# Kernel optimization log

Measured on AMD Instinct MI355X. Metric: run time of the kernel, lower is better.

The kernel has to match this reference:

```python
import jax, jax.numpy as jnp
import numpy as np

EMBED_DIM = 584
HEADS = 8
HEAD_SIZE = EMBED_DIM // HEADS  # 73
CTX = 200


def setup_inputs() -> dict:
    key = jax.random.key(0)
    ks = jax.random.split(key, 6)
    B, T = 256, 200
    x = jax.random.normal(ks[0], (B, T, EMBED_DIM), dtype=jnp.float32)
    s = 1.0 / np.sqrt(EMBED_DIM)
    # per-head q/k/v Linear(EMBED_DIM, HEAD_SIZE, bias=False) weights, stacked: [H, hs, E]
    Wq = jax.random.uniform(ks[1], (HEADS, HEAD_SIZE, EMBED_DIM), jnp.float32, -s, s)
    Wk = jax.random.uniform(ks[2], (HEADS, HEAD_SIZE, EMBED_DIM), jnp.float32, -s, s)
    Wv = jax.random.uniform(ks[3], (HEADS, HEAD_SIZE, EMBED_DIM), jnp.float32, -s, s)
    Wo = jax.random.uniform(ks[4], (EMBED_DIM, EMBED_DIM), jnp.float32, -s, s)
    bo = jax.random.uniform(ks[5], (EMBED_DIM,), jnp.float32, -s, s)
    return {"x": x, "Wq": Wq, "Wk": Wk, "Wv": Wv, "Wo": Wo, "bo": bo}


def reference(x, Wq, Wk, Wv, Wo, bo):
    B, T, C = x.shape  # C == EMBED_DIM
    # per-head projections, batched: [B, H, T, hs]
    q = jnp.einsum('bte,hfe->bhtf', x, Wq)
    k = jnp.einsum('bte,hfe->bhtf', x, Wk)
    v = jnp.einsum('bte,hfe->bhtf', x, Wv)
    # NOTE: original scales by EMBED_DIM**-0.5 (C), not head_size**-0.5
    scores = jnp.einsum('bhtf,bhsf->bhts', q, k) * (C ** -0.5)
    causal = jnp.tril(jnp.ones((T, T), dtype=bool))
    scores = jnp.where(causal, scores, -jnp.inf)
    w = jax.nn.softmax(scores, axis=-1)
    out = jnp.einsum('bhts,bhsf->bhtf', w, v)  # [B,H,T,hs]
    out = out.transpose(0, 2, 1, 3).reshape(B, T, C)  # concat heads on last dim
    return out @ Wo.T + bo
```

## Files before the change

### kernel.cpp

```cpp
#include <hip/hip_runtime.h>

typedef __bf16 bf16x8 __attribute__((ext_vector_type(8)));
typedef __bf16 bf16x4 __attribute__((ext_vector_type(4)));
typedef float f32x4 __attribute__((ext_vector_type(4)));

#define EMBED 584
#define KP 608
#define HEADS 8
#define HS 73
#define HSQ 80
#define CTX 200
#define NBATCH 256
#define MROWS 51200
#define NQKV 1752

#define CH 112
#define KSS 104
#define VTS 136
#define PSS 136

__device__ __forceinline__ void gld_lds16(__bf16* lds, const __bf16* g) {
  __builtin_amdgcn_global_load_lds(
      (const __attribute__((address_space(1))) void*)g,
      (__attribute__((address_space(3))) void*)lds, 16, 0, 0);
}

__global__ __launch_bounds__(256) void cvt_x(const float* __restrict__ x,
                                             __bf16* __restrict__ out) {
  int i = blockIdx.x * 256 + threadIdx.x;
  int r = i / 76, slot = i - r * 76;
  int col = slot * 8;
  bf16x8 o8 = {};
  if (col < EMBED) {
    const float4* s4 = (const float4*)(x + (size_t)r * EMBED + col);
    float4 f0 = s4[0], f1 = s4[1];
    o8[0] = (__bf16)f0.x; o8[1] = (__bf16)f0.y; o8[2] = (__bf16)f0.z; o8[3] = (__bf16)f0.w;
    o8[4] = (__bf16)f1.x; o8[5] = (__bf16)f1.y; o8[6] = (__bf16)f1.z; o8[7] = (__bf16)f1.w;
  }
  *(bf16x8*)(out + (size_t)r * KP + col) = o8;
}

__global__ __launch_bounds__(256) void pack_w(const float* __restrict__ Wq,
                                              const float* __restrict__ Wk,
                                              const float* __restrict__ Wv,
                                              const float* __restrict__ Wo,
                                              __bf16* __restrict__ out) {
  int i = blockIdx.x * 256 + threadIdx.x;
  if (i >= 2336 * 76) return;
  int r = i / 76, slot = i - r * 76;
  int col = slot * 8;
  bf16x8 o8 = {};
  if (col < EMBED) {
    const float* src = r < 584  ? Wq + (size_t)r * EMBED
                     : r < 1168 ? Wk + (size_t)(r - 584) * EMBED
                     : r < 1752 ? Wv + (size_t)(r - 1168) * EMBED
                                : Wo + (size_t)(r - 1752) * EMBED;
    const float4* s4 = (const float4*)(src + col);
    float4 f0 = s4[0], f1 = s4[1];
    o8[0] = (__bf16)f0.x; o8[1] = (__bf16)f0.y; o8[2] = (__bf16)f0.z; o8[3] = (__bf16)f0.w;
    o8[4] = (__bf16)f1.x; o8[5] = (__bf16)f1.y; o8[6] = (__bf16)f1.z; o8[7] = (__bf16)f1.w;
  }
  *(bf16x8*)(out + (size_t)r * KP + col) = o8;
}

__global__ __launch_bounds__(256) void gemm_qkv(const __bf16* __restrict__ A,
                                                const __bf16* __restrict__ Bm,
                                                __bf16* __restrict__ Q,
                                                __bf16* __restrict__ Ko,
                                                __bf16* __restrict__ V) {
  __shared__ __bf16 As[2][4096];
  __shared__ __bf16 Bs[2][4096];
  int tid = threadIdx.x;
  int id = blockIdx.x;
  int idp = (id & 7) * 700 + (id >> 3);
  int bm = idp / 14, bn = idp - bm * 14;
  int wid = tid >> 6, lane = tid & 63;
  int wm = (wid & 1) * 64, wn = (wid >> 1) * 64;
  int lr = lane & 15, lq = lane >> 4;
  const __bf16* aB = A  + (size_t)(bm * 128 + wid * 32 + (lane >> 2)) * KP + (lane & 3) * 8;
  const __bf16* bB = Bm + (size_t)(bn * 128 + wid * 32 + (lane >> 2)) * KP + (lane & 3) * 8;
  f32x4 acc[4][4] = {};
  gld_lds16(As[0] + wid * 1024,       aB);
  gld_lds16(As[0] + wid * 1024 + 512, aB + 16 * KP);
  gld_lds16(Bs[0] + wid * 1024,       bB);
  gld_lds16(Bs[0] + wid * 1024 + 512, bB + 16 * KP);
  __syncthreads();
  int cur = 0;
  for (int kt = 0; kt < 19; ++kt) {
    if (kt < 18) {
      int k0 = (kt + 1) * 32;
      gld_lds16(As[cur ^ 1] + wid * 1024,       aB + k0);
      gld_lds16(As[cur ^ 1] + wid * 1024 + 512, aB + 16 * KP + k0);
      gld_lds16(Bs[cur ^ 1] + wid * 1024,       bB + k0);
      gld_lds16(Bs[cur ^ 1] + wid * 1024 + 512, bB + 16 * KP + k0);
    }
    bf16x8 af[4], bfr[4];
#pragma unroll
    for (int i = 0; i < 4; ++i)
      af[i] = *(const bf16x8*)&As[cur][(wm + i * 16 + lr) * 32 + lq * 8];
#pragma unroll
    for (int j = 0; j < 4; ++j)
      bfr[j] = *(const bf16x8*)&Bs[cur][(wn + j * 16 + lr) * 32 + lq * 8];
#pragma unroll
    for (int i = 0; i < 4; ++i)
#pragma unroll
      for (int j = 0; j < 4; ++j)
        acc[i][j] = __builtin_amdgcn_mfma_f32_16x16x32_bf16(af[i], bfr[j], acc[i][j], 0, 0, 0);
    if (kt < 18) __syncthreads();
    cur ^= 1;
  }
  int whichj[4], ojv[4];
  __bf16* Pj[4];
  bool okj[4];
#pragma unroll
  for (int j = 0; j < 4; ++j) {
    int n = bn * 128 + wn + j * 16 + lr;
    okj[j] = (n < NQKV);
    int nn = okj[j] ? n : 0;
    int which = nn / EMBED;
    int rem = nn - which * EMBED;
    int hh = rem / HS;
    int f = rem - hh * HS;
    whichj[j] = which;
    ojv[j] = (which == 2) ? (hh * 16000 + f * 200) : (hh * 16000 + f);
    Pj[j] = (which == 0) ? Q : (which == 1) ? Ko : V;
  }
#pragma unroll
  for (int i = 0; i < 4; ++i) {
    int m0 = bm * 128 + wm + i * 16 + lq * 4;
    int bb = m0 / CTX;
    int tt = m0 - bb * CTX;
    int a_qk = bb * 128000 + tt * 80;
    int a_v  = bb * 128000 + tt;
#pragma unroll
    for (int j = 0; j < 4; ++j) {
      if (!okj[j]) continue;
      if (whichj[j] == 2) {
        bf16x4 v4;
#pragma unroll
        for (int r = 0; r < 4; ++r) v4[r] = (__bf16)acc[i][j][r];
        *(bf16x4*)&Pj[j][a_v + ojv[j]] = v4;
      } else {
        int base = a_qk + ojv[j];
#pragma unroll
        for (int r = 0; r < 4; ++r)
          Pj[j][base + r * 80] = (__bf16)acc[i][j][r];
      }
    }
  }
}

__global__ __launch_bounds__(256) void attn_kernel(const __bf16* __restrict__ q,
                                                   const __bf16* __restrict__ k,
                                                   const __bf16* __restrict__ v,
                                                   __bf16* __restrict__ o) {
  __shared__ __align__(16) __bf16 lds[31232];
  __bf16* Ks = lds;
  __bf16* Vt = lds + 11648;
  __bf16* Ps = lds + 22528;

  int tid = threadIdx.x;
  int bh = blockIdx.x;
  int b = bh >> 3, h = bh & 7;
  const __bf16* qg = q + (size_t)bh * (CTX * HSQ);
  const __bf16* kg = k + (size_t)bh * (CTX * HSQ);
  const __bf16* vg = v + (size_t)bh * (HSQ * CTX);

  {
    f32x4* p = (f32x4*)lds;
    for (int i = tid; i < 3904; i += 256) p[i] = f32x4{0.f, 0.f, 0.f, 0.f};
  }
  if (h == 0) {
    bf16x8 z = {};
    for (int i = tid; i < CTX * 3; i += 256) {
      int t = i / 3, seg = i - t * 3;
      *(bf16x8*)&o[((size_t)(b * CTX + t)) * KP + EMBED + seg * 8] = z;
    }
  }
  __syncthreads();

  int wid = tid >> 6, lane = tid & 63;
  int lr = lane & 15, g = lane >> 4;
  __bf16* Pw = Ps + wid * (16 * PSS);
  const int nstr = (wid == 0) ? 4 : 3;
  const float scale = 0.04138029443264672f;

  float ml[4][4], ll[4][4];
  f32x4 ov[4][5];
#pragma unroll
  for (int i = 0; i < 4; ++i)
#pragma unroll
    for (int r = 0; r < 4; ++r) { ml[i][r] = -1e30f; ll[i][r] = 0.f; }
#pragma unroll
  for (int i = 0; i < 4; ++i)
#pragma unroll
    for (int nt = 0; nt < 5; ++nt) ov[i][nt] = f32x4{0.f, 0.f, 0.f, 0.f};

  for (int c = 0; c < 2; ++c) {
    int key0 = c * CH;
    for (int idx = tid; idx < CH * 10; idx += 256) {
      int s = idx / 10, slot = idx % 10;
      int key = key0 + s;
      if (key < CTX)
        *(bf16x8*)&Ks[s * KSS + slot * 8] =
            *(const bf16x8*)&kg[(size_t)key * HSQ + slot * 8];
    }
    for (int idx = tid; idx < HSQ * 14; idx += 256) {
      int f = idx / 14, slot = idx % 14;
      int s0 = slot * 8;
      bf16x8 vv;
      if (key0 + s0 + 7 < CTX) {
        vv = *(const bf16x8*)&vg[(size_t)f * CTX + key0 + s0];
      } else {
#pragma unroll
        for (int j = 0; j < 8; ++j)
          vv[j] = (key0 + s0 + j < CTX) ? vg[(size_t)f * CTX + key0 + s0 + j]
                                        : (__bf16)0.f;
      }
      *(bf16x8*)&Vt[f * VTS + s0] = vv;
    }
    __syncthreads();

#pragma unroll
    for (int i = 0; i < 4; ++i) {
      if (i >= nstr) break;
      int strip = wid + 4 * i;
      int row0 = strip * 16;
      bf16x8 qf[3];
      qf[0] = *(const bf16x8*)&qg[(size_t)(row0 + lr) * HSQ + g * 8];
      qf[1] = *(const bf16x8*)&qg[(size_t)(row0 + lr) * HSQ + 32 + g * 8];
      if (g < 2)
        qf[2] = *(const bf16x8*)&qg[(size_t)(row0 + lr) * HSQ + 64 + g * 8];
      else
        qf[2] = bf16x8{};
      float sc[7][4];
#pragma unroll
      for (int nt = 0; nt < 7; ++nt) {
        f32x4 acc = {};
#pragma unroll
        for (int kc = 0; kc < 3; ++kc) {
          bf16x8 kf = *(const bf16x8*)&Ks[(nt * 16 + lr) * KSS + kc * 32 + g * 8];
          acc = __builtin_amdgcn_mfma_f32_16x16x32_bf16(qf[kc], kf, acc, 0, 0, 0);
        }
        int kcol = key0 + nt * 16 + lr;
#pragma unroll
        for (int r = 0; r < 4; ++r) {
          int qrow = row0 + g * 4 + r;
          sc[nt][r] = (kcol <= qrow && kcol < CTX) ? acc[r] * scale : -1e30f;
        }
      }
      float mc[4];
#pragma unroll
      for (int r = 0; r < 4; ++r) {
        float m = sc[0][r];
#pragma unroll
        for (int nt = 1; nt < 7; ++nt) m = fmaxf(m, sc[nt][r]);
        mc[r] = m;
      }
#pragma unroll
      for (int off = 8; off; off >>= 1)
#pragma unroll
        for (int r = 0; r < 4; ++r)
          mc[r] = fmaxf(mc[r], __shfl_xor(mc[r], off, 64));
      float alpha[4], rs[4];
#pragma unroll
      for (int r = 0; r < 4; ++r) {
        float mnew = fmaxf(ml[i][r], mc[r]);
        alpha[r] = __expf(ml[i][r] - mnew);
        ml[i][r] = mnew;
        float s = 0.f;
#pragma unroll
        for (int nt = 0; nt < 7; ++nt) {
          sc[nt][r] = __expf(sc[nt][r] - mnew);
          s += sc[nt][r];
        }
        rs[r] = s;
      }
#pragma unroll
      for (int off = 8; off; off >>= 1)
#pragma unroll
        for (int r = 0; r < 4; ++r) rs[r] += __shfl_xor(rs[r], off, 64);
#pragma unroll
      for (int r = 0; r < 4; ++r) ll[i][r] = ll[i][r] * alpha[r] + rs[r];
#pragma unroll
      for (int nt = 0; nt < 5; ++nt)
#pragma unroll
        for (int r = 0; r < 4; ++r) ov[i][nt][r] *= alpha[r];
#pragma unroll
      for (int nt = 0; nt < 7; ++nt)
#pragma unroll
        for (int r = 0; r < 4; ++r)
          Pw[(g * 4 + r) * PSS + nt * 16 + lr] = (__bf16)sc[nt][r];
#pragma unroll
      for (int kc = 0; kc < 4; ++kc) {
        bf16x8 pf = *(const bf16x8*)&Pw[lr * PSS + kc * 32 + g * 8];
#pragma unroll
        for (int nt = 0; nt < 5; ++nt) {
          bf16x8 vf = *(const bf16x8*)&Vt[(nt * 16 + lr) * VTS + kc * 32 + g * 8];
          ov[i][nt] = __builtin_amdgcn_mfma_f32_16x16x32_bf16(pf, vf, ov[i][nt], 0, 0, 0);
        }
      }
    }
    __syncthreads();
  }
#pragma unroll
  for (int i = 0; i < 4; ++i) {
    if (i >= nstr) break;
    int strip = wid + 4 * i;
    float inv[4];
#pragma unroll
    for (int r = 0; r < 4; ++r) inv[r] = 1.0f / ll[i][r];
#pragma unroll
    for (int nt = 0; nt < 5; ++nt) {
      int f = nt * 16 + lr;
      if (f < HS) {
#pragma unroll
        for (int r = 0; r < 4; ++r) {
          int t = strip * 16 + g * 4 + r;
          if (t < CTX)
            o[((size_t)(b * CTX + t)) * KP + h * HS + f] =
                (__bf16)(ov[i][nt][r] * inv[r]);
        }
      }
    }
  }
}

__global__ __launch_bounds__(256) void gemm_out(const __bf16* __restrict__ A,
                                                const __bf16* __restrict__ Bm,
                                                const float* __restrict__ bias,
                                                float* __restrict__ C) {
  constexpr int N = EMBED;
  __shared__ __bf16 As[2][4096];
  __shared__ __bf16 Bs[2][4096];
  int tid = threadIdx.x;
  int id = blockIdx.x;
  int idp = (id & 7) * 250 + (id >> 3);
  int bm = idp / 5, bn = idp - bm * 5;
  int wid = tid >> 6, lane = tid & 63;
  int wm = (wid & 1) * 64, wn = (wid >> 1) * 64;
  int lr = lane & 15, lq = lane >> 4;
  const __bf16* aB = A  + (size_t)(bm * 128 + wid * 32 + (lane >> 2)) * KP + (lane & 3) * 8;
  const __bf16* bB = Bm + (size_t)(bn * 128 + wid * 32 + (lane >> 2)) * KP + (lane & 3) * 8;
  f32x4 acc[4][4] = {};
  gld_lds16(As[0] + wid * 1024,       aB);
  gld_lds16(As[0] + wid * 1024 + 512, aB + 16 * KP);
  gld_lds16(Bs[0] + wid * 1024,       bB);
  gld_lds16(Bs[0] + wid * 1024 + 512, bB + 16 * KP);
  __syncthreads();
  int cur = 0;
  for (int kt = 0; kt < 19; ++kt) {
    if (kt < 18) {
      int k0 = (kt + 1) * 32;
      gld_lds16(As[cur ^ 1] + wid * 1024,       aB + k0);
      gld_lds16(As[cur ^ 1] + wid * 1024 + 512, aB + 16 * KP + k0);
      gld_lds16(Bs[cur ^ 1] + wid * 1024,       bB + k0);
      gld_lds16(Bs[cur ^ 1] + wid * 1024 + 512, bB + 16 * KP + k0);
    }
    bf16x8 af[4], bfr[4];
#pragma unroll
    for (int i = 0; i < 4; ++i)
      af[i] = *(const bf16x8*)&As[cur][(wm + i * 16 + lr) * 32 + lq * 8];
#pragma unroll
    for (int j = 0; j < 4; ++j)
      bfr[j] = *(const bf16x8*)&Bs[cur][(wn + j * 16 + lr) * 32 + lq * 8];
#pragma unroll
    for (int i = 0; i < 4; ++i)
#pragma unroll
      for (int j = 0; j < 4; ++j)
        acc[i][j] = __builtin_amdgcn_mfma_f32_16x16x32_bf16(af[i], bfr[j], acc[i][j], 0, 0, 0);
    if (kt < 18) __syncthreads();
    cur ^= 1;
  }
#pragma unroll
  for (int i = 0; i < 4; ++i) {
    int m = bm * 128 + wm + i * 16 + lq * 4;
#pragma unroll
    for (int j = 0; j < 4; ++j) {
      int n = bn * 128 + wn + j * 16 + lr;
      if (n < N) {
        float bval = bias[n];
#pragma unroll
        for (int r = 0; r < 4; ++r)
          C[(size_t)(m + r) * N + n] = acc[i][j][r] + bval;
      }
    }
  }
}

extern "C" void kernel_launch(void* const* d_in, const int* in_sizes, int n_in,
                              void* d_out, int out_size, void* d_ws, size_t ws_size,
                              hipStream_t stream) {
  const float* x  = (const float*)d_in[0];
  const float* Wq = (const float*)d_in[1];
  const float* Wk = (const float*)d_in[2];
  const float* Wv = (const float*)d_in[3];
  const float* Wo = (const float*)d_in[4];
  const float* bo = (const float*)d_in[5];
  float* out = (float*)d_out;

  __bf16* xb   = (__bf16*)d_ws;
  __bf16* wcat = xb + 31129600ULL;
  __bf16* qb   = wcat + 1420288ULL;
  __bf16* kb   = qb + 32768000ULL;
  __bf16* vb   = kb + 32768000ULL;
  __bf16* ab   = xb;

  cvt_x<<<15200, 256, 0, stream>>>(x, xb);
  pack_w<<<694, 256, 0, stream>>>(Wq, Wk, Wv, Wo, wcat);
  gemm_qkv<<<5600, 256, 0, stream>>>(xb, wcat, qb, kb, vb);
  attn_kernel<<<2048, 256, 0, stream>>>(qb, kb, vb, ab);
  gemm_out<<<2000, 256, 0, stream>>>(ab, wcat + 1752ULL * KP, bo, out);
}
```

Measured before the change: 728.7 us.

## Restructure attention to full-row softmax with causal tile skipping and direct global K/V reads

The attention kernel no longer stages K and V in LDS in two key chunks with online softmax. Each wave now processes whole query strips, computing scores only for key tiles at or below the diagonal, doing a single-pass softmax, and reading K/V fragments straight from global memory. Strips are assigned in a balanced order, LDS use shrinks to the P buffer with a 4-blocks occupancy hint, and a new kernel pre-zeroes the padded Q/K/V regions so out-of-range loads are safe. This saves masked MFMA work and block-wide syncs, at the risk of higher register pressure and uncoalesced global loads for K/V.

Result: faster. 684.0 us (-6.1%).

```diff
diff --git a/kernel.cpp b/kernel.cpp
--- a/kernel.cpp
+++ b/kernel.cpp
@@ -14,10 +14,7 @@
 #define MROWS 51200
 #define NQKV 1752
 
-#define CH 112
-#define KSS 104
-#define VTS 136
-#define PSS 136
+#define PSS 232
 
 __device__ __forceinline__ void gld_lds16(__bf16* lds, const __bf16* g) {
   __builtin_amdgcn_global_load_lds(
@@ -61,6 +58,21 @@
     o8[4] = (__bf16)f1.x; o8[5] = (__bf16)f1.y; o8[6] = (__bf16)f1.z; o8[7] = (__bf16)f1.w;
   }
   *(bf16x8*)(out + (size_t)r * KP + col) = o8;
+}
+
+__global__ __launch_bounds__(256) void zero_pads(__bf16* __restrict__ qb,
+                                                 __bf16* __restrict__ kb,
+                                                 __bf16* __restrict__ vb) {
+  int bh = blockIdx.x;
+  bf16x8 z = {};
+  __bf16* qp = qb + (size_t)bh * 16000;
+  __bf16* kp = kb + (size_t)bh * 16000;
+  __bf16* vp = vb + (size_t)bh * 16000;
+  for (int i = threadIdx.x; i < 575; i += 256) {
+    if (i < 200)      *(bf16x8*)&qp[i * 80 + 72] = z;
+    else if (i < 400) *(bf16x8*)&kp[(i - 200) * 80 + 72] = z;
+    else              *(bf16x8*)&vp[14600 + (i - 400) * 8] = z;
+  }
 }
 
 __global__ __launch_bounds__(256) void gemm_qkv(const __bf16* __restrict__ A,
@@ -150,26 +162,18 @@
   }
 }
 
-__global__ __launch_bounds__(256) void attn_kernel(const __bf16* __restrict__ q,
-                                                   const __bf16* __restrict__ k,
-                                                   const __bf16* __restrict__ v,
-                                                   __bf16* __restrict__ o) {
-  __shared__ __align__(16) __bf16 lds[31232];
-  __bf16* Ks = lds;
-  __bf16* Vt = lds + 11648;
-  __bf16* Ps = lds + 22528;
-
+__global__ __launch_bounds__(256, 4) void attn_kernel(const __bf16* __restrict__ q,
+                                                      const __bf16* __restrict__ k,
+                                                      const __bf16* __restrict__ v,
+                                                      __bf16* __restrict__ o) {
+  __shared__ __align__(16) __bf16 Ps[4][16 * PSS];
   int tid = threadIdx.x;
   int bh = blockIdx.x;
   int b = bh >> 3, h = bh & 7;
-  const __bf16* qg = q + (size_t)bh * (CTX * HSQ);
-  const __bf16* kg = k + (size_t)bh * (CTX * HSQ);
-  const __bf16* vg = v + (size_t)bh * (HSQ * CTX);
-
-  {
-    f32x4* p = (f32x4*)lds;
-    for (int i = tid; i < 3904; i += 256) p[i] = f32x4{0.f, 0.f, 0.f, 0.f};
-  }
+  const __bf16* qg = q + (size_t)bh * 16000;
+  const __bf16* kg = k + (size_t)bh * 16000;
+  const __bf16* vg = v + (size_t)bh * 16000;
+
   if (h == 0) {
     bf16x8 z = {};
     for (int i = tid; i < CTX * 3; i += 256) {
@@ -177,149 +181,113 @@
       *(bf16x8*)&o[((size_t)(b * CTX + t)) * KP + EMBED + seg * 8] = z;
     }
   }
-  __syncthreads();
 
   int wid = tid >> 6, lane = tid & 63;
   int lr = lane & 15, g = lane >> 4;
-  __bf16* Pw = Ps + wid * (16 * PSS);
-  const int nstr = (wid == 0) ? 4 : 3;
+  __bf16* Pw = Ps[wid];
   const float scale = 0.04138029443264672f;
 
-  float ml[4][4], ll[4][4];
-  f32x4 ov[4][5];
-#pragma unroll
-  for (int i = 0; i < 4; ++i)
-#pragma unroll
-    for (int r = 0; r < 4; ++r) { ml[i][r] = -1e30f; ll[i][r] = 0.f; }
-#pragma unroll
-  for (int i = 0; i < 4; ++i)
-#pragma unroll
-    for (int nt = 0; nt < 5; ++nt) ov[i][nt] = f32x4{0.f, 0.f, 0.f, 0.f};
-
-  for (int c = 0; c < 2; ++c) {
-    int key0 = c * CH;
-    for (int idx = tid; idx < CH * 10; idx += 256) {
-      int s = idx / 10, slot = idx % 10;
-      int key = key0 + s;
-      if (key < CTX)
-        *(bf16x8*)&Ks[s * KSS + slot * 8] =
-            *(const bf16x8*)&kg[(size_t)key * HSQ + slot * 8];
-    }
-    for (int idx = tid; idx < HSQ * 14; idx += 256) {
-      int f = idx / 14, slot = idx % 14;
-      int s0 = slot * 8;
-      bf16x8 vv;
-      if (key0 + s0 + 7 < CTX) {
-        vv = *(const bf16x8*)&vg[(size_t)f * CTX + key0 + s0];
-      } else {
-#pragma unroll
-        for (int j = 0; j < 8; ++j)
-          vv[j] = (key0 + s0 + j < CTX) ? vg[(size_t)f * CTX + key0 + s0 + j]
-                                        : (__bf16)0.f;
-      }
-      *(bf16x8*)&Vt[f * VTS + s0] = vv;
-    }
-    __syncthreads();
-
-#pragma unroll
-    for (int i = 0; i < 4; ++i) {
-      if (i >= nstr) break;
-      int strip = wid + 4 * i;
-      int row0 = strip * 16;
-      bf16x8 qf[3];
-      qf[0] = *(const bf16x8*)&qg[(size_t)(row0 + lr) * HSQ + g * 8];
-      qf[1] = *(const bf16x8*)&qg[(size_t)(row0 + lr) * HSQ + 32 + g * 8];
-      if (g < 2)
-        qf[2] = *(const bf16x8*)&qg[(size_t)(row0 + lr) * HSQ + 64 + g * 8];
-      else
-        qf[2] = bf16x8{};
-      float sc[7][4];
-#pragma unroll
-      for (int nt = 0; nt < 7; ++nt) {
-        f32x4 acc = {};
-#pragma unroll
-        for (int kc = 0; kc < 3; ++kc) {
-          bf16x8 kf = *(const bf16x8*)&Ks[(nt * 16 + lr) * KSS + kc * 32 + g * 8];
-          acc = __builtin_amdgcn_mfma_f32_16x16x32_bf16(qf[kc], kf, acc, 0, 0, 0);
-        }
-        int kcol = key0 + nt * 16 + lr;
-#pragma unroll
-        for (int r = 0; r < 4; ++r) {
-          int qrow = row0 + g * 4 + r;
-          sc[nt][r] = (kcol <= qrow && kcol < CTX) ? acc[r] * scale : -1e30f;
-        }
-      }
-      float mc[4];
+  int sl[4];
+  sl[0] = 12 - wid;
+  sl[1] = (wid < 3) ? 6 + wid : 5;
+  sl[2] = (wid < 3) ? 1 + wid : 4;
+  sl[3] = (wid < 3) ? -1 : 0;
+
+#pragma unroll
+  for (int si = 0; si < 4; ++si) {
+    int s = sl[si];
+    if (s < 0) continue;
+    int row0 = s * 16;
+    bf16x8 qf[3];
+    qf[0] = *(const bf16x8*)&qg[(size_t)(row0 + lr) * HSQ + g * 8];
+    qf[1] = *(const bf16x8*)&qg[(size_t)(row0 + lr) * HSQ + 32 + g * 8];
+    qf[2] = (g < 2) ? *(const bf16x8*)&qg[(size_t)(row0 + lr) * HSQ + 64 + g * 8]
+                    : bf16x8{};
+    float sc[13][4];
+#pragma unroll
+    for (int nt = 0; nt < 13; ++nt) {
+      if (nt > s) continue;
+      f32x4 acc = {};
+#pragma unroll
+      for (int kc = 0; kc < 3; ++kc) {
+        bf16x8 kf = *(const bf16x8*)&kg[(size_t)(nt * 16 + lr) * HSQ + kc * 32 + g * 8];
+        acc = __builtin_amdgcn_mfma_f32_16x16x32_bf16(qf[kc], kf, acc, 0, 0, 0);
+      }
 #pragma unroll
       for (int r = 0; r < 4; ++r) {
-        float m = sc[0][r];
-#pragma unroll
-        for (int nt = 1; nt < 7; ++nt) m = fmaxf(m, sc[nt][r]);
-        mc[r] = m;
-      }
-#pragma unroll
-      for (int off = 8; off; off >>= 1)
-#pragma unroll
-        for (int r = 0; r < 4; ++r)
-          mc[r] = fmaxf(mc[r], __shfl_xor(mc[r], off, 64));
-      float alpha[4], rs[4];
-#pragma unroll
-      for (int r = 0; r < 4; ++r) {
-        float mnew = fmaxf(ml[i][r], mc[r]);
-        alpha[r] = __expf(ml[i][r] - mnew);
-        ml[i][r] = mnew;
-        float s = 0.f;
-#pragma unroll
-        for (int nt = 0; nt < 7; ++nt) {
-          sc[nt][r] = __expf(sc[nt][r] - mnew);
-          s += sc[nt][r];
-        }
-        rs[r] = s;
-      }
-#pragma unroll
-      for (int off = 8; off; off >>= 1)
-#pragma unroll
-        for (int r = 0; r < 4; ++r) rs[r] += __shfl_xor(rs[r], off, 64);
-#pragma unroll
-      for (int r = 0; r < 4; ++r) ll[i][r] = ll[i][r] * alpha[r] + rs[r];
-#pragma unroll
-      for (int nt = 0; nt < 5; ++nt)
-#pragma unroll
-        for (int r = 0; r < 4; ++r) ov[i][nt][r] *= alpha[r];
-#pragma unroll
-      for (int nt = 0; nt < 7; ++nt)
-#pragma unroll
-        for (int r = 0; r < 4; ++r)
-          Pw[(g * 4 + r) * PSS + nt * 16 + lr] = (__bf16)sc[nt][r];
-#pragma unroll
-      for (int kc = 0; kc < 4; ++kc) {
-        bf16x8 pf = *(const bf16x8*)&Pw[lr * PSS + kc * 32 + g * 8];
-#pragma unroll
-        for (int nt = 0; nt < 5; ++nt) {
-          bf16x8 vf = *(const bf16x8*)&Vt[(nt * 16 + lr) * VTS + kc * 32 + g * 8];
-          ov[i][nt] = __builtin_amdgcn_mfma_f32_16x16x32_bf16(pf, vf, ov[i][nt], 0, 0, 0);
-        }
-      }
-    }
-    __syncthreads();
-  }
-#pragma unroll
-  for (int i = 0; i < 4; ++i) {
-    if (i >= nstr) break;
-    int strip = wid + 4 * i;
+        float val = acc[r] * scale;
+        if (nt == s && lr > g * 4 + r) val = -1e30f;
+        if (nt * 16 + lr >= CTX) val = -1e30f;
+        sc[nt][r] = val;
+      }
+    }
+    float mr[4], rs[4];
+#pragma unroll
+    for (int r = 0; r < 4; ++r) {
+      float m = -1e30f;
+#pragma unroll
+      for (int nt = 0; nt < 13; ++nt)
+        if (nt <= s) m = fmaxf(m, sc[nt][r]);
+      mr[r] = m;
+    }
+#pragma unroll
+    for (int off = 8; off; off >>= 1)
+#pragma unroll
+      for (int r = 0; r < 4; ++r)
+        mr[r] = fmaxf(mr[r], __shfl_xor(mr[r], off, 64));
+#pragma unroll
+    for (int r = 0; r < 4; ++r) {
+      float ssum = 0.f;
+#pragma unroll
+      for (int nt = 0; nt < 13; ++nt) {
+        if (nt > s) continue;
+        sc[nt][r] = __expf(sc[nt][r] - mr[r]);
+        ssum += sc[nt][r];
+      }
+      rs[r] = ssum;
+    }
+#pragma unroll
+    for (int off = 8; off; off >>= 1)
+#pragma unroll
+      for (int r = 0; r < 4; ++r) rs[r] += __shfl_xor(rs[r], off, 64);
+#pragma unroll
+    for (int nt = 0; nt < 13; ++nt) {
+      if (nt > s) continue;
+#pragma unroll
+      for (int r = 0; r < 4; ++r)
+        Pw[(g * 4 + r) * PSS + nt * 16 + lr] = (__bf16)sc[nt][r];
+    }
+    if ((s & 1) == 0) {
+#pragma unroll
+      for (int r = 0; r < 4; ++r)
+        Pw[(g * 4 + r) * PSS + (s + 1) * 16 + lr] = (__bf16)0.f;
+    }
+    f32x4 ov[5];
+#pragma unroll
+    for (int nt = 0; nt < 5; ++nt) ov[nt] = f32x4{0.f, 0.f, 0.f, 0.f};
+#pragma unroll
+    for (int kc = 0; kc < 7; ++kc) {
+      if (kc > s / 2) continue;
+      bf16x8 pf = *(const bf16x8*)&Pw[lr * PSS + kc * 32 + g * 8];
+#pragma unroll
+      for (int nt = 0; nt < 5; ++nt) {
+        bf16x8 vf = *(const bf16x8*)&vg[(size_t)(nt * 16 + lr) * CTX + kc * 32 + g * 8];
+        ov[nt] = __builtin_amdgcn_mfma_f32_16x16x32_bf16(pf, vf, ov[nt], 0, 0, 0);
+      }
+    }
     float inv[4];
 #pragma unroll
-    for (int r = 0; r < 4; ++r) inv[r] = 1.0f / ll[i][r];
+    for (int r = 0; r < 4; ++r) inv[r] = 1.0f / rs[r];
 #pragma unroll
     for (int nt = 0; nt < 5; ++nt) {
       int f = nt * 16 + lr;
       if (f < HS) {
 #pragma unroll
         for (int r = 0; r < 4; ++r) {
-          int t = strip * 16 + g * 4 + r;
+          int t = row0 + g * 4 + r;
           if (t < CTX)
             o[((size_t)(b * CTX + t)) * KP + h * HS + f] =
-                (__bf16)(ov[i][nt][r] * inv[r]);
+                (__bf16)(ov[nt][r] * inv[r]);
         }
       }
     }
@@ -399,15 +367,16 @@
   const float* bo = (const float*)d_in[5];
   float* out = (float*)d_out;
 
-  __bf16* xb   = (__bf16*)d_ws;
-  __bf16* wcat = xb + 31129600ULL;
-  __bf16* qb   = wcat + 1420288ULL;
+  __bf16* wcat = (__bf16*)d_ws;
+  __bf16* vb   = wcat + 1420288ULL;
+  __bf16* qb   = vb + 32768000ULL;
   __bf16* kb   = qb + 32768000ULL;
-  __bf16* vb   = kb + 32768000ULL;
+  __bf16* xb   = kb + 32768000ULL;
   __bf16* ab   = xb;
 
   cvt_x<<<15200, 256, 0, stream>>>(x, xb);
   pack_w<<<694, 256, 0, stream>>>(Wq, Wk, Wv, Wo, wcat);
+  zero_pads<<<2048, 256, 0, stream>>>(qb, kb, vb);
   gemm_qkv<<<5600, 256, 0, stream>>>(xb, wcat, qb, kb, vb);
   attn_kernel<<<2048, 256, 0, stream>>>(qb, kb, vb, ab);
   gemm_out<<<2000, 256, 0, stream>>>(ab, wcat + 1752ULL * KP, bo, out);
```
